# Performance work log

Hardware: AMD Instinct MI355X
Metric: run time of the kernel (lower is better)

Reference implementation:

```python
import jax, jax.numpy as jnp
import numpy as np
import math

B, S, D, HD = 8, 2048, 768, 64  # batch, seq, emb_hidden_dim, head_dim


def setup_inputs() -> dict:
    key = jax.random.key(0)
    ks = jax.random.split(key, 7)
    scale_w = 1.0 / math.sqrt(D)
    return {
        "X": jax.random.normal(ks[0], (B, S, D), dtype=jnp.float32),
        "Wq": jax.random.normal(ks[1], (D, HD), dtype=jnp.float32) * scale_w,
        "bq": jax.random.normal(ks[2], (HD,), dtype=jnp.float32) * 0.01,
        "Wk": jax.random.normal(ks[3], (D, HD), dtype=jnp.float32) * scale_w,
        "bk": jax.random.normal(ks[4], (HD,), dtype=jnp.float32) * 0.01,
        "Wv": jax.random.normal(ks[5], (D, HD), dtype=jnp.float32) * scale_w,
        "bv": jax.random.normal(ks[6], (HD,), dtype=jnp.float32) * 0.01,
    }


def reference(X, Wq, bq, Wk, bk, Wv, bv):
    # Projections: [B,S,D] @ [D,HD] -> [B,S,HD]
    Q = X @ Wq + bq
    K = X @ Wk + bk
    V = X @ Wv + bv
    # NOTE: original divides by sqrt(hidden_dim)=sqrt(D), not sqrt(head_dim)
    inv_scale = 1.0 / math.sqrt(D)
    scores = jnp.einsum("bqd,bkd->bqk", Q, K) * inv_scale  # [B,S,S]
    causal = jnp.tril(jnp.ones((S, S), dtype=bool))
    scores = jnp.where(causal, scores, -jnp.inf)
    attn = jax.nn.softmax(scores, axis=-1)
    # dropout p=0.0 (eval/deterministic reference)
    return jnp.einsum("bqk,bkd->bqd", attn, V)  # [B,S,HD]
```

## Files before the change

### kernel.cpp

```cpp
#include <hip/hip_runtime.h>
#include <hip/hip_bf16.h>
#include <math.h>

typedef __attribute__((ext_vector_type(8))) short short8;
typedef __attribute__((ext_vector_type(4))) float f32x4;

#define SS 2048
#define DD 768
#define HDIM 64
#define MM 16384

__device__ __forceinline__ short f2bf(float f) {
    union { float f; unsigned u; } v; v.f = f;
    unsigned r = (v.u + 0x7fffu + ((v.u >> 16) & 1u)) >> 16;
    return (short)r;
}
__device__ __forceinline__ float bf2f(short s) {
    union { float f; unsigned u; } v;
    v.u = ((unsigned)(unsigned short)s) << 16;
    return v.f;
}

__device__ __forceinline__ void gl_lds(const void* g, void* l) {
    __builtin_amdgcn_global_load_lds(
        (const __attribute__((address_space(1))) unsigned*)g,
        (__attribute__((address_space(3))) unsigned*)l, 16, 0, 0);
}

__global__ void prep_w(const float* __restrict__ Wq, const float* __restrict__ Wk,
                       const float* __restrict__ Wv, short* __restrict__ Wt) {
    int idx = blockIdx.x * 256 + threadIdx.x;
    int col = idx / DD;
    int k   = idx - col * DD;
    const float* W = (col < 64) ? Wq : (col < 128) ? Wk : Wv;
    int c = col & 63;
    Wt[idx] = f2bf(W[k * HDIM + c]);
}

__global__ __launch_bounds__(512)
void proj_qkv(const float* __restrict__ X, const short* __restrict__ Wt,
              const float* __restrict__ bq, const float* __restrict__ bk,
              const float* __restrict__ bv,
              short* __restrict__ Qg, short* __restrict__ Kg, short* __restrict__ Vt) {
    __shared__ float Xl[2][2048];
    __shared__ short Wl[2][12288];
    const int tid = threadIdx.x;
    const int w = tid >> 6, lane = tid & 63;
    const int lr = lane & 15, lg = lane >> 4;
    const int wr = w >> 2, wc = w & 3;
    const int row0 = blockIdx.x * 32;

    f32x4 acc[3];
    #pragma unroll
    for (int cf = 0; cf < 3; cf++) acc[cf] = (f32x4)0.0f;

    auto stage = [&](int kk, int buf) {
        {
            int o = w * 1024 + lane * 16;
            int row = o >> 8, ch = (o >> 4) & 15;
            const char* src = (const char*)X + (size_t)(row0 + row) * 3072
                              + kk * 256 + ((ch ^ (row & 7)) << 4);
            gl_lds(src, (char*)&Xl[buf][0] + w * 1024);
        }
        #pragma unroll
        for (int s = 0; s < 3; s++) {
            int i = w * 3 + s;
            int o = i * 1024 + lane * 16;
            int col = o >> 7, ch = (o >> 4) & 7;
            const char* src = (const char*)Wt + (size_t)col * 1536
                              + kk * 128 + ((ch ^ (col & 7)) << 4);
            gl_lds(src, (char*)&Wl[buf][0] + i * 1024);
        }
    };

    stage(0, 0);
    __syncthreads();
    int buf = 0;
    for (int kk = 0; kk < 12; kk++) {
        if (kk < 11) stage(kk + 1, buf ^ 1);
        const char* xb = (const char*)&Xl[buf][0];
        const char* wb = (const char*)&Wl[buf][0];
        #pragma unroll
        for (int ksub = 0; ksub < 2; ksub++) {
            int r = wr * 16 + lr;
            int b0 = r * 256 + ksub * 128 + lg * 32;
            f32x4 x0 = *(const f32x4*)(xb + ((b0)      ^ ((r & 7) << 4)));
            f32x4 x1 = *(const f32x4*)(xb + ((b0 + 16) ^ ((r & 7) << 4)));
            short8 a;
            a[0]=f2bf(x0[0]); a[1]=f2bf(x0[1]); a[2]=f2bf(x0[2]); a[3]=f2bf(x0[3]);
            a[4]=f2bf(x1[0]); a[5]=f2bf(x1[1]); a[6]=f2bf(x1[2]); a[7]=f2bf(x1[3]);
            #pragma unroll
            for (int cf = 0; cf < 3; cf++) {
                int col = wc * 48 + cf * 16 + lr;
                short8 bfr = *(const short8*)(wb +
                    ((col * 128 + ksub * 64 + lg * 16) ^ ((col & 7) << 4)));
                acc[cf] = __builtin_amdgcn_mfma_f32_16x16x32_bf16(a, bfr, acc[cf], 0, 0, 0);
            }
        }
        __syncthreads();
        buf ^= 1;
    }

    #pragma unroll
    for (int cf = 0; cf < 3; cf++) {
        int gcol = wc * 48 + cf * 16 + lr;
        int m = gcol >> 6, cc = gcol & 63;
        float bias = (m == 0 ? bq : m == 1 ? bk : bv)[cc];
        #pragma unroll
        for (int i = 0; i < 4; i++) {
            int r = row0 + wr * 16 + lg * 4 + i;
            short o = f2bf(acc[cf][i] + bias);
            if (m == 0)      Qg[(size_t)r * HDIM + cc] = o;
            else if (m == 1) Kg[(size_t)r * HDIM + cc] = o;
            else             Vt[(size_t)cc * MM + r]   = o;
        }
    }
}

__global__ __launch_bounds__(512)
void attn_part(const short* __restrict__ Qg, const short* __restrict__ Kg,
               const short* __restrict__ Vt,
               short* __restrict__ Opart, float* __restrict__ Ml,
               float* __restrict__ out) {
    __shared__ short Kl[2][4096];
    __shared__ short Vl[2][4096];
    __shared__ short Pl[8][1024];
    const int tid = threadIdx.x;
    const int w = tid >> 6, lane = tid & 63;
    const int lr = lane & 15, lg = lane >> 4;
    const int b = (int)blockIdx.x & 7;
    const int cidx = (int)blockIdx.x >> 3;

    int r0 = 95 - cidx;
    int J = 0, acc0 = 0;
    while (r0 >= acc0 + (2 * J + 4) / 3) { acc0 += (2 * J + 4) / 3; J++; }
    const int c = r0 - acc0;
    const int t0 = 3 * c;
    const int t1 = min(2 * J + 2, 3 * c + 3);

    const int q0 = J * 128 + w * 16;
    char* plbase = (char*)&Pl[w][0];

    short8 qf[2];
    qf[0] = *(const short8*)(Qg + ((size_t)b * SS + q0 + lr) * HDIM + lg * 8);
    qf[1] = *(const short8*)(Qg + ((size_t)b * SS + q0 + lr) * HDIM + 32 + lg * 8);

    f32x4 oacc[4];
    #pragma unroll
    for (int d = 0; d < 4; d++) oacc[d] = (f32x4)0.0f;
    float mrow[4] = {-INFINITY, -INFINITY, -INFINITY, -INFINITY};
    float lrow[4] = {0.f, 0.f, 0.f, 0.f};
    const float scl = 0.03608439182435161f;

    auto stage = [&](int t, int buf) {
        const int kv0 = t * 64;
        {
            int o = w * 1024 + lane * 16;
            int row = o >> 7, ch = (o >> 4) & 7;
            const char* src = (const char*)Kg + ((size_t)b * SS + kv0) * 128
                              + row * 128 + ((ch ^ (row & 7)) << 4);
            gl_lds(src, (char*)&Kl[buf][0] + w * 1024);
        }
        {
            int o = w * 1024 + lane * 16;
            int col = o >> 7, ch = (o >> 4) & 7;
            const char* src = (const char*)Vt + (size_t)col * (MM * 2)
                              + ((size_t)b * SS + kv0) * 2 + ((ch ^ (col & 7)) << 4);
            gl_lds(src, (char*)&Vl[buf][0] + w * 1024);
        }
    };

    stage(t0, 0);
    __syncthreads();
    int buf = 0;
    for (int t = t0; t < t1; t++) {
        if (t + 1 < t1) stage(t + 1, buf ^ 1);
        const int kv0 = t * 64;
        const bool active = (kv0 <= q0 + 15);
        if (active) {
            const char* kb = (const char*)&Kl[buf][0];
            f32x4 sacc[4];
            #pragma unroll
            for (int ct = 0; ct < 4; ct++) sacc[ct] = (f32x4)0.0f;
            #pragma unroll
            for (int ct = 0; ct < 4; ct++) {
                int row = ct * 16 + lr;
                short8 k0 = *(const short8*)(kb + ((row * 128 +      lg * 16) ^ ((row & 7) << 4)));
                short8 k1 = *(const short8*)(kb + ((row * 128 + 64 + lg * 16) ^ ((row & 7) << 4)));
                sacc[ct] = __builtin_amdgcn_mfma_f32_16x16x32_bf16(qf[0], k0, sacc[ct], 0, 0, 0);
                sacc[ct] = __builtin_amdgcn_mfma_f32_16x16x32_bf16(qf[1], k1, sacc[ct], 0, 0, 0);
            }

            const bool maskt = (kv0 + 63 > q0);
            float p[4][4];
            float rm[4] = {-1e30f, -1e30f, -1e30f, -1e30f};
            #pragma unroll
            for (int ct = 0; ct < 4; ct++) {
                #pragma unroll
                for (int i = 0; i < 4; i++) {
                    float s = sacc[ct][i] * scl;
                    if (maskt) {
                        int kv = kv0 + ct * 16 + lr;
                        int qr = q0 + lg * 4 + i;
                        if (kv > qr) s = -1e30f;
                    }
                    p[ct][i] = s;
                    rm[i] = fmaxf(rm[i], s);
                }
            }
            #pragma unroll
            for (int i = 0; i < 4; i++) {
                float v = rm[i];
                v = fmaxf(v, __shfl_xor(v, 1));
                v = fmaxf(v, __shfl_xor(v, 2));
                v = fmaxf(v, __shfl_xor(v, 4));
                v = fmaxf(v, __shfl_xor(v, 8));
                rm[i] = v;
            }
            float rs[4];
            #pragma unroll
            for (int i = 0; i < 4; i++) {
                float mn = fmaxf(mrow[i], rm[i]);
                float scale = __expf(mrow[i] - mn);
                mrow[i] = mn;
                lrow[i] *= scale;
                for (int d = 0; d < 4; d++) oacc[d][i] *= scale;
                float sum = 0.f;
                #pragma unroll
                for (int ct = 0; ct < 4; ct++) {
                    float e = __expf(p[ct][i] - mn);
                    p[ct][i] = e;
                    sum += e;
                }
                rs[i] = sum;
            }
            #pragma unroll
            for (int i = 0; i < 4; i++) {
                float v = rs[i];
                v += __shfl_xor(v, 1);
                v += __shfl_xor(v, 2);
                v += __shfl_xor(v, 4);
                v += __shfl_xor(v, 8);
                lrow[i] += v;
            }

            #pragma unroll
            for (int ct = 0; ct < 4; ct++) {
                #pragma unroll
                for (int i = 0; i < 4; i++) {
                    int r = lg * 4 + i;
                    int byteoff = r * 128 + (ct * 16 + lr) * 2;
                    *(short*)(plbase + (byteoff ^ ((r & 7) << 4))) = f2bf(p[ct][i]);
                }
            }

            const char* vb = (const char*)&Vl[buf][0];
            #pragma unroll
            for (int ks = 0; ks < 2; ks++) {
                int byteoff = lr * 128 + ks * 64 + lg * 16;
                short8 pf = *(const short8*)(plbase + (byteoff ^ ((lr & 7) << 4)));
                #pragma unroll
                for (int d = 0; d < 4; d++) {
                    int col = d * 16 + lr;
                    short8 vf = *(const short8*)(vb +
                        ((col * 128 + ks * 64 + lg * 16) ^ ((col & 7) << 4)));
                    oacc[d] = __builtin_amdgcn_mfma_f32_16x16x32_bf16(pf, vf, oacc[d], 0, 0, 0);
                }
            }
        }
        __syncthreads();
        buf ^= 1;
    }

    if (J == 0) {
        #pragma unroll
        for (int d = 0; d < 4; d++)
            #pragma unroll
            for (int i = 0; i < 4; i++)
                out[((size_t)b * SS + q0 + lg * 4 + i) * HDIM + d * 16 + lr]
                    = oacc[d][i] / lrow[i];
    } else {
        const int pb = (b * 16 + J) * 12 + c;
        short* op = Opart + (size_t)pb * 8192 + (size_t)(w * 16) * 64;
        #pragma unroll
        for (int d = 0; d < 4; d++)
            #pragma unroll
            for (int i = 0; i < 4; i++)
                op[(lg * 4 + i) * 64 + d * 16 + lr] = f2bf(oacc[d][i]);
        if (lr == 0) {
            float* ml = Ml + (size_t)pb * 256;
            for (int i = 0; i < 4; i++) {
                ml[w * 16 + lg * 4 + i]       = mrow[i];
                ml[128 + w * 16 + lg * 4 + i] = lrow[i];
            }
        }
    }
}

__global__ __launch_bounds__(256)
void attn_comb(const short* __restrict__ Opart, const float* __restrict__ Ml,
               float* __restrict__ out) {
    const int b = (int)blockIdx.x & 7;
    const int J = ((int)blockIdx.x >> 3) + 1;
    const int nc = (2 * J + 4) / 3;
    const int tid = threadIdx.x;
    const int r = tid >> 1, h = tid & 1;
    const int base = (b * 16 + J) * 12;

    float m = -INFINITY;
    for (int c = 0; c < nc; c++) m = fmaxf(m, Ml[(size_t)(base + c) * 256 + r]);

    float L = 0.f;
    f32x4 acc[8];
    #pragma unroll
    for (int q = 0; q < 8; q++) acc[q] = (f32x4)0.0f;
    for (int c = 0; c < nc; c++) {
        const float* ml = Ml + (size_t)(base + c) * 256;
        float sc = __expf(ml[r] - m);
        L += ml[128 + r] * sc;
        const short* op = Opart + (size_t)(base + c) * 8192 + r * 64 + h * 32;
        #pragma unroll
        for (int q = 0; q < 4; q++) {
            short8 s = *(const short8*)(op + q * 8);
            f32x4 lo = {bf2f(s[0]), bf2f(s[1]), bf2f(s[2]), bf2f(s[3])};
            f32x4 hi = {bf2f(s[4]), bf2f(s[5]), bf2f(s[6]), bf2f(s[7])};
            acc[q * 2]     += lo * sc;
            acc[q * 2 + 1] += hi * sc;
        }
    }
    float inv = 1.0f / L;
    float* o = out + ((size_t)b * SS + J * 128 + r) * HDIM + h * 32;
    #pragma unroll
    for (int q = 0; q < 8; q++) {
        f32x4 v = acc[q] * inv;
        *(f32x4*)(o + q * 4) = v;
    }
}

extern "C" void kernel_launch(void* const* d_in, const int* in_sizes, int n_in,
                              void* d_out, int out_size, void* d_ws, size_t ws_size,
                              hipStream_t stream) {
    const float* X  = (const float*)d_in[0];
    const float* Wq = (const float*)d_in[1];
    const float* bq = (const float*)d_in[2];
    const float* Wk = (const float*)d_in[3];
    const float* bk = (const float*)d_in[4];
    const float* Wv = (const float*)d_in[5];
    const float* bv = (const float*)d_in[6];
    float* out = (float*)d_out;

    char* ws = (char*)d_ws;
    short* Wt = (short*)(ws);
    short* Qg = (short*)(ws + 294912);
    short* Kg = (short*)(ws + 294912 + 2097152);
    short* Vt = (short*)(ws + 294912 + 2 * 2097152);
    size_t opOff = 294912 + 3 * (size_t)2097152;
    short* Op = (short*)(ws + opOff);
    float* Ml = (float*)(ws + opOff + (size_t)1536 * 8192 * 2);

    prep_w<<<576, 256, 0, stream>>>(Wq, Wk, Wv, Wt);
    proj_qkv<<<512, 512, 0, stream>>>(X, Wt, bq, bk, bv, Qg, Kg, Vt);
    attn_part<<<768, 512, 0, stream>>>(Qg, Kg, Vt, Op, Ml, out);
    attn_comb<<<120, 256, 0, stream>>>(Op, Ml, out);
}
```

Baseline: 57.77 us.

## Load X directly into registers in QKV projection and halve block rows

The projection kernel no longer stages X through LDS. Each lane now loads its fp32 X fragment straight from global memory into registers and prefetches the next k-step while the current one computes. Blocks shrink to 16 rows and 4 waves, so there are twice as many blocks and each wave covers 48 output columns. This removes LDS traffic and LDS space for X, at the cost of per-block W staging being amortised over fewer rows and more register pressure from the prefetch buffers.

```diff
diff --git a/kernel.cpp b/kernel.cpp
--- a/kernel.cpp
+++ b/kernel.cpp
@@ -37,34 +37,25 @@
     Wt[idx] = f2bf(W[k * HDIM + c]);
 }
 
-__global__ __launch_bounds__(512)
+__global__ __launch_bounds__(256)
 void proj_qkv(const float* __restrict__ X, const short* __restrict__ Wt,
               const float* __restrict__ bq, const float* __restrict__ bk,
               const float* __restrict__ bv,
               short* __restrict__ Qg, short* __restrict__ Kg, short* __restrict__ Vt) {
-    __shared__ float Xl[2][2048];
     __shared__ short Wl[2][12288];
     const int tid = threadIdx.x;
     const int w = tid >> 6, lane = tid & 63;
     const int lr = lane & 15, lg = lane >> 4;
-    const int wr = w >> 2, wc = w & 3;
-    const int row0 = blockIdx.x * 32;
+    const int row0 = blockIdx.x * 16;
 
     f32x4 acc[3];
     #pragma unroll
     for (int cf = 0; cf < 3; cf++) acc[cf] = (f32x4)0.0f;
 
-    auto stage = [&](int kk, int buf) {
-        {
-            int o = w * 1024 + lane * 16;
-            int row = o >> 8, ch = (o >> 4) & 15;
-            const char* src = (const char*)X + (size_t)(row0 + row) * 3072
-                              + kk * 256 + ((ch ^ (row & 7)) << 4);
-            gl_lds(src, (char*)&Xl[buf][0] + w * 1024);
-        }
-        #pragma unroll
-        for (int s = 0; s < 3; s++) {
-            int i = w * 3 + s;
+    auto stageW = [&](int kk, int buf) {
+        #pragma unroll
+        for (int s = 0; s < 6; s++) {
+            int i = w * 6 + s;
             int o = i * 1024 + lane * 16;
             int col = o >> 7, ch = (o >> 4) & 7;
             const char* src = (const char*)Wt + (size_t)col * 1536
@@ -72,26 +63,31 @@
             gl_lds(src, (char*)&Wl[buf][0] + i * 1024);
         }
     };
-
-    stage(0, 0);
+    auto loadX = [&](int kk, f32x4* xr) {
+        const float* p = X + (size_t)(row0 + lr) * DD + kk * 64 + lg * 8;
+        xr[0] = *(const f32x4*)(p);
+        xr[1] = *(const f32x4*)(p + 4);
+        xr[2] = *(const f32x4*)(p + 32);
+        xr[3] = *(const f32x4*)(p + 36);
+    };
+
+    f32x4 xc[4], xn[4];
+    stageW(0, 0);
+    loadX(0, xc);
     __syncthreads();
     int buf = 0;
     for (int kk = 0; kk < 12; kk++) {
-        if (kk < 11) stage(kk + 1, buf ^ 1);
-        const char* xb = (const char*)&Xl[buf][0];
+        if (kk < 11) { stageW(kk + 1, buf ^ 1); loadX(kk + 1, xn); }
         const char* wb = (const char*)&Wl[buf][0];
         #pragma unroll
         for (int ksub = 0; ksub < 2; ksub++) {
-            int r = wr * 16 + lr;
-            int b0 = r * 256 + ksub * 128 + lg * 32;
-            f32x4 x0 = *(const f32x4*)(xb + ((b0)      ^ ((r & 7) << 4)));
-            f32x4 x1 = *(const f32x4*)(xb + ((b0 + 16) ^ ((r & 7) << 4)));
+            f32x4 x0 = xc[ksub * 2], x1 = xc[ksub * 2 + 1];
             short8 a;
             a[0]=f2bf(x0[0]); a[1]=f2bf(x0[1]); a[2]=f2bf(x0[2]); a[3]=f2bf(x0[3]);
             a[4]=f2bf(x1[0]); a[5]=f2bf(x1[1]); a[6]=f2bf(x1[2]); a[7]=f2bf(x1[3]);
             #pragma unroll
             for (int cf = 0; cf < 3; cf++) {
-                int col = wc * 48 + cf * 16 + lr;
+                int col = w * 48 + cf * 16 + lr;
                 short8 bfr = *(const short8*)(wb +
                     ((col * 128 + ksub * 64 + lg * 16) ^ ((col & 7) << 4)));
                 acc[cf] = __builtin_amdgcn_mfma_f32_16x16x32_bf16(a, bfr, acc[cf], 0, 0, 0);
@@ -99,16 +95,18 @@
         }
         __syncthreads();
         buf ^= 1;
+        #pragma unroll
+        for (int q = 0; q < 4; q++) xc[q] = xn[q];
     }
 
     #pragma unroll
     for (int cf = 0; cf < 3; cf++) {
-        int gcol = wc * 48 + cf * 16 + lr;
+        int gcol = w * 48 + cf * 16 + lr;
         int m = gcol >> 6, cc = gcol & 63;
         float bias = (m == 0 ? bq : m == 1 ? bk : bv)[cc];
         #pragma unroll
         for (int i = 0; i < 4; i++) {
-            int r = row0 + wr * 16 + lg * 4 + i;
+            int r = row0 + lg * 4 + i;
             short o = f2bf(acc[cf][i] + bias);
             if (m == 0)      Qg[(size_t)r * HDIM + cc] = o;
             else if (m == 1) Kg[(size_t)r * HDIM + cc] = o;
@@ -359,7 +357,7 @@
     float* Ml = (float*)(ws + opOff + (size_t)1536 * 8192 * 2);
 
     prep_w<<<576, 256, 0, stream>>>(Wq, Wk, Wv, Wt);
-    proj_qkv<<<512, 512, 0, stream>>>(X, Wt, bq, bk, bv, Qg, Kg, Vt);
+    proj_qkv<<<1024, 256, 0, stream>>>(X, Wt, bq, bk, bv, Qg, Kg, Vt);
     attn_part<<<768, 512, 0, stream>>>(Qg, Kg, Vt, Op, Ml, out);
     attn_comb<<<120, 256, 0, stream>>>(Op, Ml, out);
 }
```

Measured after the change: 81.13 us. +40.4%, slower.
